# Optimization experiments

Measured on AMD Instinct MI355X. Metric: run time of the kernel, lower is better.

## Reference

```python
import jax, jax.numpy as jnp
import numpy as np
from jax import lax

# ---- fake-quant helpers (brevitas-style per-tensor float scaling, STE round) ----
EPS = 1e-8

def _ste_round(x):
    return x + lax.stop_gradient(jnp.round(x) - x)

def _scale(x, qmax):
    s = lax.stop_gradient(jnp.max(jnp.abs(x))) / qmax
    return jnp.maximum(s, EPS)

def fq(x, scale, qmin, qmax):
    # fake-quantize: round-to-nearest with straight-through estimator, clip, dequant
    return jnp.clip(_ste_round(x / scale), qmin, qmax) * scale

def quant_act_int8(x):
    s = _scale(x, 127.0)
    return fq(x, s, -128.0, 127.0), s

def quant_weight_int4(w):
    # 4-bit signed, narrow range [-7, 7] (brevitas weight quant default narrow_range)
    s = _scale(w, 7.0)
    return fq(w, s, -7.0, 7.0), s

def quant_relu_uint4(x):
    y = jax.nn.relu(x)
    s = _scale(y, 15.0)
    return fq(y, s, 0.0, 15.0)

def quant_bias_int32(b, scale):
    # Int32Bias: bias quantized at input_scale * weight_scale
    return _ste_round(b / scale) * scale

def conv2d_same(x, w):
    # NCHW, OIHW, padding=1, stride=1
    return lax.conv_general_dilated(x, w, window_strides=(1, 1), padding=((1, 1), (1, 1)),
                                    dimension_numbers=('NCHW', 'OIHW', 'NCHW'))

def maxpool2(x):
    return lax.reduce_window(x, -jnp.inf, lax.max, (1, 1, 2, 2), (1, 1, 2, 2), 'VALID')

def quant_conv(x, w, b):
    xq, sx = quant_act_int8(x)        # input_quant: Int8ActPerTensorFloat
    wq, sw = quant_weight_int4(w)     # weight_bit_width=4
    bq = quant_bias_int32(b, sx * sw) # bias_quant: Int32Bias
    y = conv2d_same(xq, wq) + bq[None, :, None, None]
    yq, _ = quant_act_int8(y)         # output_quant: Int8ActPerTensorFloat
    return yq

def quant_linear(x, w, b):
    xq, sx = quant_act_int8(x)
    wq, sw = quant_weight_int4(w)
    bq = quant_bias_int32(b, sx * sw)
    y = xq @ wq.T + bq
    yq, _ = quant_act_int8(y)
    return yq


def setup_inputs() -> dict:
    key = jax.random.key(0)
    ks = jax.random.split(key, 7)
    B = 8192
    x = jax.random.normal(ks[0], (B, 1, 28, 28), dtype=jnp.float32)
    w1 = jax.random.normal(ks[1], (16, 1, 3, 3), dtype=jnp.float32) * 0.3
    b1 = jax.random.normal(ks[2], (16,), dtype=jnp.float32) * 0.1
    w2 = jax.random.normal(ks[3], (32, 16, 3, 3), dtype=jnp.float32) * 0.1
    b2 = jax.random.normal(ks[4], (32,), dtype=jnp.float32) * 0.1
    wf = jax.random.normal(ks[5], (10, 32 * 7 * 7), dtype=jnp.float32) * 0.05
    bf = jax.random.normal(ks[6], (10,), dtype=jnp.float32) * 0.1
    return {'x': x, 'w1': w1, 'b1': b1, 'w2': w2, 'b2': b2, 'wf': wf, 'bf': bf}


def reference(x, w1, b1, w2, b2, wf, bf):
    h, _ = quant_act_int8(x)              # inputQuant
    h = quant_conv(h, w1, b1)             # conv1
    h = quant_relu_uint4(h)               # relu1 (4-bit)
    h = maxpool2(h)                       # pool1 -> [B,16,14,14]
    h = quant_conv(h, w2, b2)             # conv2
    h = quant_relu_uint4(h)               # relu2
    h = maxpool2(h)                       # pool2 -> [B,32,7,7]
    h = h.reshape(h.shape[0], -1)         # flatten -> [B,1568]
    return quant_linear(h, wf, bf)        # fc -> [B,10]
```

## Files before the change

### kernel.cpp

```cpp
#include <hip/hip_runtime.h>
#include <climits>

#define NB 8192
#define EPSQ 1e-8f

using i32x4  = __attribute__((ext_vector_type(4)))  int;
using i32x16 = __attribute__((ext_vector_type(16))) int;

#define WS_F(ws)     ((float*)(ws))
#define WS_I(ws)     ((int*)((char*)(ws)+128))
#define WS_B1L(ws)   ((int*)((char*)(ws)+384))
#define WS_B2L(ws)   ((int*)((char*)(ws)+448))
#define WS_BFL(ws)   ((int*)((char*)(ws)+576))
#define WS_M1F(ws)   ((float*)((char*)(ws)+640))
#define WS_B1F(ws)   ((float*)((char*)(ws)+1280))
#define WS_B2FR(ws)  ((char*)(ws)+2048)
#define WS_Q2TAB(ws) ((signed char*)((char*)(ws)+7168))
#define WS_Q3TAB(ws) ((signed char*)((char*)(ws)+7424))
#define WS_B1FR(ws)  ((char*)(ws)+7680)
#define WS_MFF(ws)   ((float*)((char*)(ws)+20480))
#define WS_WFP(ws)   ((char*)(ws)+83200)
#define WS_RA1(ws)   ((int*)((char*)(ws)+139264))
#define WS_RS1(ws)   ((int*)((char*)(ws)+164352))
#define WS_RA2(ws)   ((int*)((char*)(ws)+189440))
#define WS_RS2(ws)   ((int*)((char*)(ws)+197632))
#define WS_RA3(ws)   ((int*)((char*)(ws)+205824))
#define WS_RAX(ws)   ((float*)((char*)(ws)+206848))
#define WS_WMX(ws)   ((float*)((char*)(ws)+215040))
#define WS_BIG_OFF   217088

__device__ __forceinline__ float clampf(float v, float lo, float hi){ return fminf(fmaxf(v, lo), hi); }

__device__ __forceinline__ float wave_max_f(float v){
#pragma unroll
  for (int off=32; off; off>>=1) v = fmaxf(v, __shfl_down(v, off, 64));
  return v;
}
__device__ __forceinline__ int wave_max_i(int v){
#pragma unroll
  for (int off=32; off; off>>=1) v = max(v, __shfl_down(v, off, 64));
  return v;
}

__device__ __forceinline__ void reduce2_atomic(int amax, int smax, int* gA, int* gS){
  amax = wave_max_i(amax); smax = wave_max_i(smax);
  __shared__ int sA[4], sS[4];
  int w = threadIdx.x>>6, l = threadIdx.x&63;
  if (l==0){ sA[w]=amax; sS[w]=smax; }
  __syncthreads();
  if (threadIdx.x==0){
#pragma unroll
    for (int i=1;i<4;i++){ amax=max(amax,sA[i]); smax=max(smax,sS[i]); }
    atomicMax(gA, amax); atomicMax(gS, smax);
  }
}

__device__ __forceinline__ void reduce2_store(int amax, int smax, int* pA, int* pS){
  amax = wave_max_i(amax); smax = wave_max_i(smax);
  __shared__ int sA[4], sS[4];
  int w = threadIdx.x>>6, l = threadIdx.x&63;
  if (l==0){ sA[w]=amax; sS[w]=smax; }
  __syncthreads();
  if (threadIdx.x==0){
#pragma unroll
    for (int i=1;i<4;i++){ amax=max(amax,sA[i]); smax=max(smax,sS[i]); }
    *pA = amax; *pS = smax;
  }
}

__global__ void k_init(char* ws){
  int* I = WS_I(ws);
  if (threadIdx.x==0){ I[0]=0; I[1]=0; I[2]=INT_MIN; I[3]=0; I[4]=INT_MIN; I[5]=0; }
}

__global__ void k_absx(const float* __restrict__ x, char* ws){
  const float4* x4 = (const float4*)x;
  const int n4 = NB*784/4;
  float m = 0.f;
  for (int i = blockIdx.x*blockDim.x + threadIdx.x; i < n4; i += gridDim.x*blockDim.x){
    float4 v = x4[i];
    m = fmaxf(m, fmaxf(fmaxf(fabsf(v.x),fabsf(v.y)), fmaxf(fabsf(v.z),fabsf(v.w))));
  }
  m = wave_max_f(m);
  __shared__ float sm[4];
  int w = threadIdx.x>>6;
  if ((threadIdx.x&63)==0) sm[w]=m;
  __syncthreads();
  if (threadIdx.x==0){
    m = fmaxf(fmaxf(sm[0],sm[1]), fmaxf(sm[2],sm[3]));
    WS_RAX(ws)[blockIdx.x] = m;
  }
}

__global__ void k_wmax(const float* __restrict__ w1, const float* __restrict__ w2,
                       const float* __restrict__ wf, char* ws){
  __shared__ float red[256];
  int b = blockIdx.x, t = threadIdx.x;
  float m = 0.f;
  if (b==0){ if (t<144) m = fabsf(w1[t]); }
  else if (b<19){ m = fabsf(w2[(b-1)*256 + t]); }
  else { int i=(b-19)*256+t; if (i<15680) m = fabsf(wf[i]); }
  red[t]=m; __syncthreads();
  for (int s=128;s;s>>=1){ if (t<s) red[t]=fmaxf(red[t],red[t+s]); __syncthreads(); }
  if (t==0) WS_WMX(ws)[b]=red[0];
}

__global__ void k_scales(const float* __restrict__ w1, const float* __restrict__ b1, char* ws){
  __shared__ float red[256];
  float* F = WS_F(ws);
  int t = threadIdx.x;
  float vw1 = WS_WMX(ws)[0];
  float m2=0.f, mf=0.f;
  if (t<18) m2 = WS_WMX(ws)[1+t];
  if (t<62) mf = WS_WMX(ws)[19+t];
  red[t]=m2; __syncthreads();
  for (int s=128;s;s>>=1){ if (t<s) red[t]=fmaxf(red[t],red[t+s]); __syncthreads(); }
  float mw2=red[0]; __syncthreads();
  red[t]=mf; __syncthreads();
  for (int s=128;s;s>>=1){ if (t<s) red[t]=fmaxf(red[t],red[t+s]); __syncthreads(); }
  float mwf=red[0]; __syncthreads();
  float mxv=0.f;
  for (int i=t;i<2048;i+=256) mxv=fmaxf(mxv,WS_RAX(ws)[i]);
  red[t]=mxv; __syncthreads();
  for (int s=128;s;s>>=1){ if (t<s) red[t]=fmaxf(red[t],red[t+s]); __syncthreads(); }
  float mx=red[0]; __syncthreads();

  float s0  = fmaxf(mx/127.f, EPSQ);
  float sx1 = fmaxf((127.f*s0)/127.f, EPSQ);
  float sw1 = fmaxf(vw1/7.f, EPSQ);
  float sw2 = fmaxf(mw2/7.f, EPSQ);
  float swf = fmaxf(mwf/7.f, EPSQ);
  float sb1 = sx1*sw1;
  if (t==0){ F[0]=s0; F[1]=sx1; F[2]=sw1; F[3]=sb1; F[7]=sw2; F[12]=swf; }
  if (t<144) WS_M1F(ws)[t] = clampf(rintf(w1[t]/sw1), -7.f, 7.f);
  if (t<16){
    int bl = (int)rintf(b1[t]/sb1);
    WS_B1L(ws)[t] = bl;
    WS_B1F(ws)[t] = (float)bl;
  }
}

__global__ void k_pack(const float* __restrict__ w1, const float* __restrict__ w2,
                       const float* __restrict__ wf, char* ws){
  const float* F = WS_F(ws);
  int id = blockIdx.x*256 + threadIdx.x;
  if (id < 5120){
    float sw2 = F[7];
    int chunk=id>>10, r=id&1023, ln=r>>4, j=r&15;
    int tap=2*chunk+(ln>>5), oc=ln&31;
    signed char v=0;
    if (tap<9) v=(signed char)clampf(rintf(w2[oc*144 + j*9 + tap]/sw2), -7.f, 7.f);
    WS_B2FR(ws)[id]=v;
  } else if (id < 6144){
    float sw1 = F[2];
    int i=id-5120;
    int ln=i>>4, j=i&15;
    int k=(ln>>5)*16+j, oc=ln&31;
    signed char v=0;
    if (k<9 && oc<16) v=(signed char)clampf(rintf(w1[oc*9+k]/sw1), -7.f, 7.f);
    WS_B1FR(ws)[i]=v;
  } else if (id < 56320){
    float swf = F[12];
    int i=id-6144;
    int chunk=i>>10, r2=i&1023, ln=r2>>4, j=r2&15;
    int oc=ln&31, k=chunk*32+(ln>>5)*16+j;
    int cell=k>>5, ch=k&31;
    signed char v=0;
    if (oc<10) v=(signed char)clampf(rintf(wf[oc*1568 + ch*49 + cell]/swf), -7.f, 7.f);
    ((signed char*)WS_WFP(ws))[i]=v;
  } else if (id < 72000){
    float swf = F[12];
    int i=id-56320;
    WS_MFF(ws)[i] = clampf(rintf(wf[i]/swf), -7.f, 7.f);
  }
}

__global__ void k_wq(const float* __restrict__ w1, const float* __restrict__ b1,
                     const float* __restrict__ w2, const float* __restrict__ wf,
                     char* ws){
  __shared__ float red[256];
  float* F = WS_F(ws);
  int t = threadIdx.x;
  auto bmaxabs = [&](const float* p, int n)->float{
    float m=0.f; for (int i=t;i<n;i+=256) m=fmaxf(m,fabsf(p[i]));
    red[t]=m; __syncthreads();
    for (int s=128;s;s>>=1){ if (t<s) red[t]=fmaxf(red[t],red[t+s]); __syncthreads(); }
    float r=red[0]; __syncthreads(); return r;
  };
  float mw1 = bmaxabs(w1,144);
  float mw2 = bmaxabs(w2,4608);
  float mwf = bmaxabs(wf,15680);
  float mxv=0.f;
  for (int i=t;i<2048;i+=256) mxv=fmaxf(mxv,WS_RAX(ws)[i]);
  red[t]=mxv; __syncthreads();
  for (int s=128;s;s>>=1){ if (t<s) red[t]=fmaxf(red[t],red[t+s]); __syncthreads(); }
  float mx=red[0]; __syncthreads();

  float s0  = fmaxf(mx/127.f, EPSQ);
  float sx1 = fmaxf((127.f*s0)/127.f, EPSQ);
  float sw1 = fmaxf(mw1/7.f, EPSQ);
  float sw2 = fmaxf(mw2/7.f, EPSQ);
  float swf = fmaxf(mwf/7.f, EPSQ);
  float sb1 = sx1*sw1;
  if (t==0){ F[0]=s0; F[1]=sx1; F[2]=sw1; F[3]=sb1; F[7]=sw2; F[12]=swf; }
  float* m1f = WS_M1F(ws);
  for (int i=t;i<144;i+=256) m1f[i] = clampf(rintf(w1[i]/sw1), -7.f, 7.f);
  if (t<16){
    int bl = (int)rintf(b1[t]/sb1);
    WS_B1L(ws)[t] = bl;
    WS_B1F(ws)[t] = (float)bl;
  }
  for (int i=t;i<5120;i+=256){
    int chunk=i>>10, r=i&1023, ln=r>>4, j=r&15;
    int tap=2*chunk+(ln>>5), oc=ln&31;
    signed char v=0;
    if (tap<9) v=(signed char)clampf(rintf(w2[oc*144 + j*9 + tap]/sw2), -7.f, 7.f);
    WS_B2FR(ws)[i]=v;
  }
  for (int i=t;i<1024;i+=256){
    int ln=i>>4, j=i&15;
    int k=(ln>>5)*16+j, oc=ln&31;
    signed char v=0;
    if (k<9 && oc<16) v=(signed char)clampf(rintf(w1[oc*9+k]/sw1), -7.f, 7.f);
    WS_B1FR(ws)[i]=v;
  }
  float* mff = WS_MFF(ws);
  for (int i=t;i<15680;i+=256) mff[i] = clampf(rintf(wf[i]/swf), -7.f, 7.f);
  for (int i=t;i<50176;i+=256){
    int chunk=i>>10, r2=i&1023, ln=r2>>4, j=r2&15;
    int oc=ln&31, k=chunk*32+(ln>>5)*16+j;
    int cell=k>>5, ch=k&31;
    signed char v=0;
    if (oc<10) v=(signed char)clampf(rintf(wf[oc*1568 + ch*49 + cell]/swf), -7.f, 7.f);
    ((signed char*)WS_WFP(ws))[i]=v;
  }
}

template<bool FULLR>
__global__ void k_s1(const float* __restrict__ b2, char* ws){
  float* F=WS_F(ws); int* I=WS_I(ws);
  __shared__ int rA[256], rS[256];
  __shared__ float sh[4];
  int t=threadIdx.x;
  int amaxI, smaxI;
  if constexpr (FULLR){
    int a=0, s=INT_MIN;
    const int* ra=WS_RA1(ws); const int* rs=WS_RS1(ws);
    for (int i=t;i<6272;i+=256){ a=max(a,ra[i]); s=max(s,rs[i]); }
    rA[t]=a; rS[t]=s; __syncthreads();
    for (int st=128;st;st>>=1){ if (t<st){ rA[t]=max(rA[t],rA[t+st]); rS[t]=max(rS[t],rS[t+st]); } __syncthreads(); }
    amaxI=rA[0]; smaxI=rS[0];
  } else { amaxI=I[1]; smaxI=I[2]; }
  if (t==0){
    float sb1=F[3];
    float sy1 = fmaxf((sb1*(float)amaxI)/127.f, EPSQ);
    float mp  = sb1*(float)smaxI;
    float P1  = clampf(rintf(mp/sy1), 0.f, 127.f);
    float sr1 = fmaxf((sy1*P1)/15.f, EPSQ);
    float N1  = clampf(rintf((sy1*P1)/sr1), 0.f, 15.f);
    float sx2 = fmaxf((N1*sr1)/127.f, EPSQ);
    float sb2 = sx2*F[7];
    F[4]=sy1; F[5]=sr1; F[6]=sx2; F[8]=sb2;
    sh[0]=sy1; sh[1]=sr1; sh[2]=sx2; sh[3]=sb2;
  }
  __syncthreads();
  float sy1=sh[0], sr1=sh[1], sx2=sh[2], sb2=sh[3];
  int k = t-128;
  float n = (k>0) ? clampf(rintf((sy1*(float)k)/sr1), 0.f, 15.f) : 0.f;
  WS_Q2TAB(ws)[t] = (signed char)clampf(rintf((n*sr1)/sx2), -128.f, 127.f);
  if (t<32) WS_B2L(ws)[t] = (int)rintf(b2[t]/sb2);
}

template<bool FULLR>
__global__ void k_s2(const float* __restrict__ bf, char* ws){
  float* F=WS_F(ws); int* I=WS_I(ws);
  __shared__ int rA[256], rS[256];
  __shared__ float sh[4];
  int t=threadIdx.x;
  int amaxI, smaxI;
  if constexpr (FULLR){
    int a=0, s=INT_MIN;
    const int* ra=WS_RA2(ws); const int* rs=WS_RS2(ws);
    for (int i=t;i<2048;i+=256){ a=max(a,ra[i]); s=max(s,rs[i]); }
    rA[t]=a; rS[t]=s; __syncthreads();
    for (int st=128;st;st>>=1){ if (t<st){ rA[t]=max(rA[t],rA[t+st]); rS[t]=max(rS[t],rS[t+st]); } __syncthreads(); }
    amaxI=rA[0]; smaxI=rS[0];
  } else { amaxI=I[3]; smaxI=I[4]; }
  if (t==0){
    float sb2=F[8];
    float sy2 = fmaxf((sb2*(float)amaxI)/127.f, EPSQ);
    float mp  = sb2*(float)smaxI;
    float P2  = clampf(rintf(mp/sy2), 0.f, 127.f);
    float sr2 = fmaxf((sy2*P2)/15.f, EPSQ);
    float N2  = clampf(rintf((sy2*P2)/sr2), 0.f, 15.f);
    float sx3 = fmaxf((N2*sr2)/127.f, EPSQ);
    float sb3 = sx3*F[12];
    F[9]=sy2; F[10]=sr2; F[11]=sx3; F[13]=sb3;
    sh[0]=sy2; sh[1]=sr2; sh[2]=sx3; sh[3]=sb3;
  }
  __syncthreads();
  float sy2=sh[0], sr2=sh[1], sx3=sh[2], sb3=sh[3];
  int k = t-128;
  float n = (k>0) ? clampf(rintf((sy2*(float)k)/sr2), 0.f, 15.f) : 0.f;
  WS_Q3TAB(ws)[t] = (signed char)clampf(rintf((n*sr2)/sx3), -128.f, 127.f);
  if (t<16) WS_BFL(ws)[t] = (t<10) ? (int)rintf(bf[t]/sb3) : 0;
}

template<bool FULLR>
__global__ void k_s3(char* ws){
  float* F=WS_F(ws); int* I=WS_I(ws);
  __shared__ int rA[256];
  int t=threadIdx.x;
  int amaxI;
  if constexpr (FULLR){
    rA[t] = WS_RA3(ws)[t];
    __syncthreads();
    for (int st=128;st;st>>=1){ if (t<st) rA[t]=max(rA[t],rA[t+st]); __syncthreads(); }
    amaxI = rA[0];
  } else { amaxI = I[5]; }
  if (t==0) F[14] = fmaxf((F[13]*(float)amaxI)/127.f, EPSQ);
}

__global__ void k_qx(const float* __restrict__ x, const char* __restrict__ ws,
                     signed char* __restrict__ qx){
  const float s0 = ((const float*)ws)[0];
  int id = blockIdx.x*256 + threadIdx.x;
  int img = id/240, w = id - img*240;
  int r = w>>3, c4 = (w&7)<<2;
  const float* xi = x + img*784;
  unsigned out = 0;
#pragma unroll
  for (int j=0;j<4;j++){
    int c = c4+j;
    bool valid = (r>=1) && (r<=28) && (c>=1) && (c<=28);
    int q = 0;
    if (valid){
      float xv = xi[(r-1)*28 + (c-1)];
      q = (int)clampf(rintf(xv/s0), -128.f, 127.f);
    }
    out |= ((unsigned)(unsigned char)(signed char)q) << (8*j);
  }
  ((unsigned*)qx)[id] = out;
}

__global__ __launch_bounds__(256) void k_conv1(const signed char* __restrict__ qx,
                                               char* __restrict__ ws,
                                               short* __restrict__ i1p){
  const int t = threadIdx.x;
  const int id = blockIdx.x*256 + t;
  const int img = id/196, cell = id - img*196;
  const int py = cell/14, px = cell - py*14;
  const signed char* qb = qx + img*960 + (2*py)*32;
  const int pc0 = 2*px;
  const int al = pc0 & ~3, sh = (pc0&3)*8;
  float in[4][4];
#pragma unroll
  for (int rr=0; rr<4; rr++){
    unsigned lo = *(const unsigned*)(qb + rr*32 + al);
    unsigned hi = *(const unsigned*)(qb + rr*32 + al + 4);
    unsigned wrd = (unsigned)(((((unsigned long long)hi)<<32)|lo) >> sh);
#pragma unroll
    for (int cc=0; cc<4; cc++)
      in[rr][cc] = (float)(signed char)((wrd >> (8*cc)) & 0xFFu);
  }
  const float* __restrict__ m1f = WS_M1F(ws);
  const float* __restrict__ b1f = WS_B1F(ws);
  int amax=0, smax=INT_MIN;
  short outv[16];
#pragma unroll
  for (int oc=0; oc<16; oc++){
    float b = b1f[oc];
    float a00=b, a01=b, a10=b, a11=b;
#pragma unroll
    for (int dy=0; dy<3; dy++){
#pragma unroll
      for (int dx=0; dx<3; dx++){
        float wt = m1f[oc*9+dy*3+dx];
        a00 = fmaf(in[dy  ][dx  ], wt, a00);
        a01 = fmaf(in[dy  ][dx+1], wt, a01);
        a10 = fmaf(in[dy+1][dx  ], wt, a10);
        a11 = fmaf(in[dy+1][dx+1], wt, a11);
      }
    }
    int v00=(int)a00, v01=(int)a01, v10=(int)a10, v11=(int)a11;
    int mx = max(max(v00,v01), max(v10,v11));
    int ax = max(max(v00<0?-v00:v00, v01<0?-v01:v01), max(v10<0?-v10:v10, v11<0?-v11:v11));
    amax = max(amax, ax);
    smax = max(smax, mx);
    outv[oc] = (short)mx;
  }
  int4* dst = (int4*)(i1p + (size_t)id*16);
  dst[0] = *(const int4*)&outv[0];
  dst[1] = *(const int4*)&outv[8];
  reduce2_store(amax, smax, &WS_RA1(ws)[blockIdx.x], &WS_RS1(ws)[blockIdx.x]);
}

__global__ __launch_bounds__(256) void k_conv2r(char* __restrict__ ws,
                                                short* __restrict__ i1p,
                                                int* __restrict__ p2g){
  __shared__ __align__(16) signed char q2p4[4][4096];
  const int t=threadIdx.x, lane=t&63, wid=t>>6;
  const int img = blockIdx.x*4 + wid;
  signed char* q2p = q2p4[wid];
  const float* F = WS_F(ws);
  const float sb1=F[3], sy1=F[4];
  const signed char* q2t = WS_Q2TAB(ws);

#pragma unroll
  for (int k=0;k<8;k++) ((unsigned long long*)q2p)[lane + 64*k] = 0ULL;

  const unsigned* src = (const unsigned*)(i1p + (size_t)img*3136);
  for (int k=0;k<25;k++){
    int idx = lane + 64*k;
    if (idx >= 1568) break;
    unsigned wv = src[idx];
    int e0 = idx*2;
    int cellc = e0 >> 4, ch = e0 & 15;
    int pyc = cellc/14, pxc = cellc - pyc*14;
    int m0 = (int)(short)(wv & 0xFFFFu);
    int m1 = (int)(short)(wv >> 16);
    float k10 = clampf(rintf((sb1*(float)m0)/sy1), -128.f, 127.f);
    float k11 = clampf(rintf((sb1*(float)m1)/sy1), -128.f, 127.f);
    int b0 = (int)(unsigned char)q2t[(int)k10+128];
    int b1 = (int)(unsigned char)q2t[(int)k11+128];
    *(unsigned short*)(q2p + ((pyc+1)*16 + (pxc+1))*16 + ch) = (unsigned short)(b0 | (b1<<8));
  }

  i32x4 bfr[5];
  const i32x4* bg = (const i32x4*)WS_B2FR(ws);
#pragma unroll
  for (int c=0;c<5;c++) bfr[c] = bg[c*64+lane];
  const int col = lane&31, h = lane>>5;
  const int bias = WS_B2L(ws)[col];
  int amax2=0, smax2=INT_MIN;
  const int TOFF[9] = {0,1,2,16,17,18,32,33,34};
  int* dstb = p2g + (size_t)img*1568;

#pragma unroll
  for (int mt=0; mt<7; mt++){
    int m = mt*32 + col;
    int g = m>>2, sub = m&3;
    bool gv = g < 49;
    int py = (g*37)>>8;
    int px = g - py*7;
    int oy = 2*py + (sub>>1), ox = 2*px + (sub&1);
    int E0 = oy*16 + ox;
    i32x16 acc;
#pragma unroll
    for (int r=0;r<16;r++) acc[r] = bias;
#pragma unroll
    for (int c=0;c<5;c++){
      const int t0 = TOFF[2*c];
      const int t1 = (2*c+1<9) ? TOFF[2*c+1] : -1;
      int toff = h ? t1 : t0;
      int entry = (gv && toff>=0) ? (E0 + toff) : 0;
      i32x4 a = *(const i32x4*)(q2p + entry*16);
      acc = __builtin_amdgcn_mfma_i32_32x32x32_i8(a, bfr[c], acc, 0,0,0);
    }
#pragma unroll
    for (int i=0;i<4;i++){
      int gg = mt*8 + 2*i + h;
      if (gg < 49){
        int v0=acc[4*i], v1=acc[4*i+1], v2=acc[4*i+2], v3=acc[4*i+3];
        int a0=v0<0?-v0:v0, a1=v1<0?-v1:v1, a2=v2<0?-v2:v2, a3=v3<0?-v3:v3;
        amax2 = max(amax2, max(max(a0,a1),max(a2,a3)));
        int mx = max(max(v0,v1),max(v2,v3));
        smax2 = max(smax2, mx);
        dstb[gg*32 + col] = mx;
      }
    }
  }
  reduce2_store(amax2, smax2, &WS_RA2(ws)[blockIdx.x], &WS_RS2(ws)[blockIdx.x]);
}

__global__ void k_rq2(const char* __restrict__ ws, const int* __restrict__ p2g,
                      signed char* __restrict__ q3g){
  const float* F = (const float*)ws;
  const float sb2 = F[8], sy2 = F[9];
  const signed char* q3t = WS_Q3TAB(ws);
  int id = blockIdx.x*256 + threadIdx.x;
  i32x4 m4 = ((const i32x4*)p2g)[id];
  unsigned out=0;
#pragma unroll
  for (int j=0;j<4;j++){
    float k2 = clampf(rintf((sb2*(float)m4[j])/sy2), -128.f, 127.f);
    out |= ((unsigned)(unsigned char)q3t[(int)k2+128]) << (8*j);
  }
  ((unsigned*)q3g)[id] = out;
}

__global__ __launch_bounds__(256) void k_fc(char* __restrict__ ws,
                                            const signed char* __restrict__ q3g,
                                            int* __restrict__ i3out){
  __shared__ int part[3][16][64];
  int t=threadIdx.x, lane=t&63, wid=t>>6;
  int mt = blockIdx.x;
  const int col=lane&31, h=lane>>5;
  const signed char* A0 = q3g + (size_t)(mt*32 + col)*1568 + 16*h;
  const i32x4* wfp = (const i32x4*)WS_WFP(ws);
  i32x16 acc;
#pragma unroll
  for (int r=0;r<16;r++) acc[r]=0;
  for (int c=wid; c<49; c+=4){
    i32x4 a = *(const i32x4*)(A0 + c*32);
    i32x4 b = wfp[c*64 + lane];
    acc = __builtin_amdgcn_mfma_i32_32x32x32_i8(a, b, acc, 0,0,0);
  }
  if (wid>0){
#pragma unroll
    for (int r=0;r<16;r++) part[wid-1][r][lane] = acc[r];
  }
  __syncthreads();
  if (wid==0){
    int bias = (col<10) ? WS_BFL(ws)[col] : 0;
    int am=0;
#pragma unroll
    for (int r=0;r<16;r++){
      int v = acc[r] + part[0][r][lane] + part[1][r][lane] + part[2][r][lane] + bias;
      int row=(r&3)+8*(r>>2)+4*h;
      int img = mt*32+row;
      if (col<10){
        i3out[img*10+col] = v;
        am = max(am, v<0?-v:v);
      }
    }
    am = wave_max_i(am);
    if (lane==0) WS_RA3(ws)[blockIdx.x] = am;
  }
}

__global__ __launch_bounds__(256) void k_c1(const float* __restrict__ x, char* __restrict__ ws,
                                            short* __restrict__ i1p){
  constexpr int OFF_K0=0, OFF_A=960, OFF_I1=13760, OFF_B1=38848;
  __shared__ __align__(16) char arena[38912];
  signed char* k0b = (signed char*)(arena+OFF_K0);
  signed char* Abuf= (signed char*)(arena+OFF_A);
  short*       I1s = (short*)(arena+OFF_I1);
  int*         b1i = (int*)(arena+OFF_B1);

  const int tid=threadIdx.x, img=blockIdx.x;
  const int lane=tid&63, wid=tid>>6;
  const float s0 = WS_F(ws)[0];

  if (tid<16) b1i[tid]=WS_B1L(ws)[tid];
  for (int i=tid;i<240;i+=256) ((int*)k0b)[i]=0;
  for (int i=tid;i<3200;i+=256) ((int*)Abuf)[i]=0;
  __syncthreads();
  const float* xi = x + img*784;
  for (int i=tid;i<784;i+=256){
    int r=i/28, c=i-r*28;
    float v = clampf(rintf(xi[i]/s0), -128.f, 127.f);
    k0b[(r+1)*32 + (c+1)] = (signed char)v;
  }
  __syncthreads();
  for (int p=tid;p<784;p+=256){
    int oy=p/28, ox=p-oy*28;
    int base = oy*32+ox;
    int al = base & ~3, sh = (base&3)*8;
    unsigned l0a=*(const unsigned*)(k0b+al),    l1a=*(const unsigned*)(k0b+al+4);
    unsigned l0b=*(const unsigned*)(k0b+al+32), l1b=*(const unsigned*)(k0b+al+36);
    unsigned l0c=*(const unsigned*)(k0b+al+64), l1c=*(const unsigned*)(k0b+al+68);
    unsigned u0=(unsigned)(((((unsigned long long)l1a)<<32)|l0a)>>sh);
    unsigned u1=(unsigned)(((((unsigned long long)l1b)<<32)|l0b)>>sh);
    unsigned u2=(unsigned)(((((unsigned long long)l1c)<<32)|l0c)>>sh);
    i32x4 row;
    row[0]=(int)((u0&0xFFFFFFu)|(u1<<24));
    row[1]=(int)(((u1>>8)&0xFFFFu)|((u2&0xFFFFu)<<16));
    row[2]=(int)((u2>>16)&0xFFu);
    row[3]=0;
    *(i32x4*)(Abuf + p*16) = row;
  }
  __syncthreads();
  const i32x4 bfr = ((const i32x4*)WS_B1FR(ws))[lane];
  const int col=lane&31, h=lane>>5;
  const int bias=(col<16)? b1i[col] : 0;
  int amax=0, smax=INT_MIN;
  for (int mt=wid; mt<25; mt+=4){
    i32x4 a={0,0,0,0};
    if (h==0) a = *(const i32x4*)(Abuf + (mt*32+col)*16);
    i32x16 acc;
#pragma unroll
    for (int r=0;r<16;r++) acc[r]=bias;
    acc=__builtin_amdgcn_mfma_i32_32x32x32_i8(a,bfr,acc,0,0,0);
#pragma unroll
    for (int r=0;r<16;r++){
      int row=(r&3)+8*(r>>2)+4*h;
      int p=mt*32+row;
      if (p<784 && col<16){
        int v=acc[r];
        amax=max(amax,v<0?-v:v); smax=max(smax,v);
        I1s[p*16+col]=(short)v;
      }
    }
  }
  __syncthreads();
  for (int i=tid;i<3136;i+=256){
    int pp=i>>4, c=i&15, py=pp/14, px=pp-py*14;
    int p0=py*56+px*2;
    int m=max(max((int)I1s[p0*16+c],(int)I1s[(p0+1)*16+c]),
              max((int)I1s[(p0+28)*16+c],(int)I1s[(p0+29)*16+c]));
    i1p[(size_t)img*3136 + i]=(short)m;
  }
  reduce2_atomic(amax,smax,&WS_I(ws)[1],&WS_I(ws)[2]);
}

template<bool FIN>
__global__ __launch_bounds__(256) void k_c2(char* __restrict__ ws, const short* __restrict__ i1p,
                                            int* __restrict__ i3out){
  constexpr int OFF_Q2L=0, OFF_B2I=3136, OFF_Q2T=3264, OFF_N2=3520,
                OFF_Q3T=9792, OFF_BFS=10048, OFF_Q3F=10112, OFF_RED=16384;
  constexpr int ARENA = FIN ? 16544 : 3520;
  __shared__ __align__(16) char arena[ARENA];
  signed char* q2l=(signed char*)(arena+OFF_Q2L);
  int* b2li=(int*)(arena+OFF_B2I);
  signed char* q2t=(signed char*)(arena+OFF_Q2T);

  const int tid=threadIdx.x, img=blockIdx.x;
  const int lane=tid&63, wid=tid>>6;
  const float* F=WS_F(ws);
  const float sb1=F[3], sy1=F[4];

  q2t[tid]=WS_Q2TAB(ws)[tid];
  if (tid<32) b2li[tid]=WS_B2L(ws)[tid];
  if constexpr (FIN){
    ((signed char*)(arena+OFF_Q3T))[tid]=WS_Q3TAB(ws)[tid];
    if (tid<16) ((int*)(arena+OFF_BFS))[tid]=WS_BFL(ws)[tid];
  }
  __syncthreads();
  for (int i=tid;i<3136;i+=256){
    int m=(int)i1p[(size_t)img*3136+i];
    float k1=clampf(rintf((sb1*(float)m)/sy1),-128.f,127.f);
    q2l[i]=q2t[(int)k1+128];
  }
  __syncthreads();

  i32x4 bfr[5];
  {
    const i32x4* bg=(const i32x4*)WS_B2FR(ws);
#pragma unroll
    for (int c=0;c<5;c++) bfr[c]=bg[c*64+lane];
  }
  const int col=lane&31, h=lane>>5;
  const int bias=b2li[col];
  int amax2=0, smax2=INT_MIN;
  float sb2=0.f, sy2=0.f;
  signed char* n2buf=nullptr;
  if constexpr (FIN){ sb2=F[8]; sy2=F[9]; n2buf=(signed char*)(arena+OFF_N2); }

  for (int mt=wid; mt<7; mt+=4){
    const int p=mt*32+col;
    const bool pv=p<196;
    const int oy=p/14, ox=p-oy*14;
    i32x16 acc;
#pragma unroll
    for (int r=0;r<16;r++) acc[r]=bias;
#pragma unroll
    for (int c=0;c<5;c++){
      const int tap=2*c+h;
      i32x4 a={0,0,0,0};
      if (pv && tap<9){
        const int iy=oy+tap/3-1, ix=ox+tap-(tap/3)*3-1;
        if ((unsigned)iy<14u && (unsigned)ix<14u) a=*(const i32x4*)(q2l+(iy*14+ix)*16);
      }
      acc=__builtin_amdgcn_mfma_i32_32x32x32_i8(a,bfr[c],acc,0,0,0);
    }
#pragma unroll
    for (int r=0;r<16;r++){
      const int row=(r&3)+8*(r>>2)+4*h;
      const int pp=mt*32+row;
      if (pp<196){
        const int v=acc[r];
        if constexpr (!FIN){ amax2=max(amax2,v<0?-v:v); smax2=max(smax2,v); }
        else {
          n2buf[col*196+pp]=(signed char)clampf(rintf((sb2*(float)v)/sy2),-128.f,127.f);
        }
      }
    }
  }
  if constexpr (!FIN){
    reduce2_atomic(amax2,smax2,&WS_I(ws)[3],&WS_I(ws)[4]);
    return;
  } else {
    __syncthreads();
    signed char* q3t_s=(signed char*)(arena+OFF_Q3T);
    float* q3f=(float*)(arena+OFF_Q3F);
    for (int i=tid;i<1568;i+=256){
      int cch=i/49, s=i-cch*49, qy=s/7, qx=s-qy*7;
      int b=cch*196+qy*28+qx*2;
      int m=max(max((int)n2buf[b],(int)n2buf[b+1]),max((int)n2buf[b+14],(int)n2buf[b+15]));
      q3f[i]=(float)q3t_s[m+128];
    }
    __syncthreads();
    const float* mff=WS_MFF(ws);
    float a10[10];
#pragma unroll
    for (int o=0;o<10;o++) a10[o]=0.f;
    for (int k=tid;k<1568;k+=256){
      float qa=q3f[k];
#pragma unroll
      for (int o=0;o<10;o++) a10[o]=fmaf(qa,mff[o*1568+k],a10[o]);
    }
#pragma unroll
    for (int o=0;o<10;o++){
#pragma unroll
      for (int off=32;off;off>>=1) a10[o]+=__shfl_down(a10[o],off,64);
    }
    float* redf=(float*)(arena+OFF_RED);
    int* bfs=(int*)(arena+OFF_BFS);
    if (lane==0){
#pragma unroll
      for (int o=0;o<10;o++) redf[wid*10+o]=a10[o];
    }
    __syncthreads();
    if (tid<10){
      float s=redf[tid]+redf[10+tid]+redf[20+tid]+redf[30+tid];
      int I3v=(int)s+bfs[tid];
      i3out[img*10+tid]=I3v;
      redf[tid]=(float)(I3v<0?-I3v:I3v);
    }
    __syncthreads();
    if (tid==0){
      int m=0;
#pragma unroll
      for (int o=0;o<10;o++) m=max(m,(int)redf[o]);
      atomicMax(&WS_I(ws)[5],m);
    }
  }
}

__global__ void k_out(char* ws, float* __restrict__ out){
  float* F=WS_F(ws);
  float sb3=F[13], sy3=F[14];
  int i = blockIdx.x*blockDim.x + threadIdx.x;
  if (i < NB*10){
    int iv = ((const int*)out)[i];
    float y = sb3*(float)iv;
    float q = clampf(rintf(y/sy3), -128.f, 127.f);
    out[i] = q*sy3;
  }
}

extern "C" void kernel_launch(void* const* d_in, const int* in_sizes, int n_in,
                              void* d_out, int out_size, void* d_ws, size_t ws_size,
                              hipStream_t stream){
  const float* x  = (const float*)d_in[0];
  const float* w1 = (const float*)d_in[1];
  const float* b1 = (const float*)d_in[2];
  const float* w2 = (const float*)d_in[3];
  const float* b2 = (const float*)d_in[4];
  const float* wf = (const float*)d_in[5];
  const float* bf = (const float*)d_in[6];
  char* ws = (char*)d_ws;
  float* out = (float*)d_out;
  int* i3 = (int*)d_out;

  const size_t QX_SZ  = (size_t)NB*960;
  const size_t I1_SZ  = (size_t)NB*6272;
  const size_t Q3_SZ  = (size_t)NB*1568;
  const size_t needFull = (size_t)WS_BIG_OFF + QX_SZ + I1_SZ + Q3_SZ;

  if (ws_size >= needFull){
    signed char* qx  = (signed char*)(ws + WS_BIG_OFF);
    short*       i1p = (short*)(ws + WS_BIG_OFF + QX_SZ);
    int*         p2g = (int*)i1p;
    signed char* q3g = (signed char*)(ws + WS_BIG_OFF + QX_SZ + I1_SZ);
    k_absx  <<<dim3(2048), dim3(256), 0, stream>>>(x, ws);
    k_wmax  <<<dim3(81), dim3(256), 0, stream>>>(w1, w2, wf, ws);
    k_scales<<<dim3(1), dim3(256), 0, stream>>>(w1, b1, ws);
    k_qx    <<<dim3(NB*240/256), dim3(256), 0, stream>>>(x, ws, qx);
    k_pack  <<<dim3(282), dim3(256), 0, stream>>>(w1, w2, wf, ws);
    k_conv1 <<<dim3(NB*196/256), dim3(256), 0, stream>>>(qx, ws, i1p);
    k_s1<true><<<dim3(1), dim3(256), 0, stream>>>(b2, ws);
    k_conv2r<<<dim3(NB/4), dim3(256), 0, stream>>>(ws, i1p, p2g);
    k_s2<true><<<dim3(1), dim3(256), 0, stream>>>(bf, ws);
    k_rq2   <<<dim3(NB*1568/1024), dim3(256), 0, stream>>>(ws, p2g, q3g);
    k_fc    <<<dim3(256), dim3(256), 0, stream>>>(ws, q3g, i3);
    k_s3<true><<<dim3(1), dim3(256), 0, stream>>>(ws);
  } else {
    short* i1p = (short*)(ws + WS_BIG_OFF);
    k_init<<<dim3(1), dim3(64), 0, stream>>>(ws);
    k_absx<<<dim3(2048), dim3(256), 0, stream>>>(x, ws);
    k_wq  <<<dim3(1), dim3(256), 0, stream>>>(w1, b1, w2, wf, ws);
    k_c1<<<dim3(NB), dim3(256), 0, stream>>>(x, ws, i1p);
    k_s1<false><<<dim3(1), dim3(256), 0, stream>>>(b2, ws);
    k_c2<false><<<dim3(NB), dim3(256), 0, stream>>>(ws, i1p, i3);
    k_s2<false><<<dim3(1), dim3(256), 0, stream>>>(bf, ws);
    k_c2<true ><<<dim3(NB), dim3(256), 0, stream>>>(ws, i1p, i3);
    k_s3<false><<<dim3(1), dim3(256), 0, stream>>>(ws);
  }
  k_out<<<dim3((NB*10+255)/256), dim3(256), 0, stream>>>(ws, out);
}
```

Measured before the change: 137.8 us.

## Fuse conv2 requant into FC, precompute int16 requant LUT, merge s3 into output

Adds a 64K-entry table that maps each possible int16 pooled conv1 value directly to its conv2 input byte, so conv2r does one lookup per element instead of float math plus a lookup. The separate requantize pass (k_rq2) is folded into the FC kernel, which requantizes its 32 images' pooled conv2 outputs into shared memory before the MFMA loop. This removes a global int8 intermediate buffer and one launch. The final scale reduction (k_s3) is merged into the output kernel, where every block redundantly reduces the 256 partial maxima. The cost is that the FC kernel now reads int32 data through a serial per-image loop and uses about 50KB of shared memory, which can lower occupancy.

```diff
diff --git a/kernel.cpp b/kernel.cpp
--- a/kernel.cpp
+++ b/kernel.cpp
@@ -27,7 +27,8 @@
 #define WS_RA3(ws)   ((int*)((char*)(ws)+205824))
 #define WS_RAX(ws)   ((float*)((char*)(ws)+206848))
 #define WS_WMX(ws)   ((float*)((char*)(ws)+215040))
-#define WS_BIG_OFF   217088
+#define WS_Q2B(ws)   ((signed char*)((char*)(ws)+215552))
+#define WS_BIG_OFF   281600
 
 __device__ __forceinline__ float clampf(float v, float lo, float hi){ return fminf(fmaxf(v, lo), hi); }
 
@@ -271,6 +272,15 @@
   if (t<32) WS_B2L(ws)[t] = (int)rintf(b2[t]/sb2);
 }
 
+__global__ void k_q2big(char* ws){
+  const float* F = WS_F(ws);
+  const float sb1=F[3], sy1=F[4];
+  int idx = blockIdx.x*256 + threadIdx.x;
+  int m = idx - 32768;
+  float k1 = clampf(rintf((sb1*(float)m)/sy1), -128.f, 127.f);
+  WS_Q2B(ws)[idx] = WS_Q2TAB(ws)[(int)k1+128];
+}
+
 template<bool FULLR>
 __global__ void k_s2(const float* __restrict__ bf, char* ws){
   float* F=WS_F(ws); int* I=WS_I(ws);
@@ -402,9 +412,7 @@
   const int t=threadIdx.x, lane=t&63, wid=t>>6;
   const int img = blockIdx.x*4 + wid;
   signed char* q2p = q2p4[wid];
-  const float* F = WS_F(ws);
-  const float sb1=F[3], sy1=F[4];
-  const signed char* q2t = WS_Q2TAB(ws);
+  const signed char* __restrict__ q2b = WS_Q2B(ws);
 
 #pragma unroll
   for (int k=0;k<8;k++) ((unsigned long long*)q2p)[lane + 64*k] = 0ULL;
@@ -419,10 +427,8 @@
     int pyc = cellc/14, pxc = cellc - pyc*14;
     int m0 = (int)(short)(wv & 0xFFFFu);
     int m1 = (int)(short)(wv >> 16);
-    float k10 = clampf(rintf((sb1*(float)m0)/sy1), -128.f, 127.f);
-    float k11 = clampf(rintf((sb1*(float)m1)/sy1), -128.f, 127.f);
-    int b0 = (int)(unsigned char)q2t[(int)k10+128];
-    int b1 = (int)(unsigned char)q2t[(int)k11+128];
+    int b0 = (int)(unsigned char)q2b[m0+32768];
+    int b1 = (int)(unsigned char)q2b[m1+32768];
     *(unsigned short*)(q2p + ((pyc+1)*16 + (pxc+1))*16 + ch) = (unsigned short)(b0 | (b1<<8));
   }
 
@@ -473,36 +479,32 @@
   reduce2_store(amax2, smax2, &WS_RA2(ws)[blockIdx.x], &WS_RS2(ws)[blockIdx.x]);
 }
 
-__global__ void k_rq2(const char* __restrict__ ws, const int* __restrict__ p2g,
-                      signed char* __restrict__ q3g){
-  const float* F = (const float*)ws;
+__global__ __launch_bounds__(256) void k_fc2(char* __restrict__ ws,
+                                             const int* __restrict__ p2g,
+                                             int* __restrict__ i3out){
+  __shared__ __align__(16) signed char q3l[32*1584];
+  __shared__ int part[3][16][64];
+  const float* F = WS_F(ws);
   const float sb2 = F[8], sy2 = F[9];
-  const signed char* q3t = WS_Q3TAB(ws);
-  int id = blockIdx.x*256 + threadIdx.x;
-  i32x4 m4 = ((const i32x4*)p2g)[id];
-  unsigned out=0;
-#pragma unroll
-  for (int j=0;j<4;j++){
-    float k2 = clampf(rintf((sb2*(float)m4[j])/sy2), -128.f, 127.f);
-    out |= ((unsigned)(unsigned char)q3t[(int)k2+128]) << (8*j);
-  }
-  ((unsigned*)q3g)[id] = out;
-}
-
-__global__ __launch_bounds__(256) void k_fc(char* __restrict__ ws,
-                                            const signed char* __restrict__ q3g,
-                                            int* __restrict__ i3out){
-  __shared__ int part[3][16][64];
+  const signed char* __restrict__ q3t = WS_Q3TAB(ws);
   int t=threadIdx.x, lane=t&63, wid=t>>6;
   int mt = blockIdx.x;
+  const int* pb = p2g + (size_t)mt*32*1568;
+  for (int il=0; il<32; il++){
+    for (int k=t; k<1568; k+=256){
+      int v = pb[il*1568 + k];
+      float k2 = clampf(rintf((sb2*(float)v)/sy2), -128.f, 127.f);
+      q3l[il*1584 + k] = q3t[(int)k2+128];
+    }
+  }
+  __syncthreads();
   const int col=lane&31, h=lane>>5;
-  const signed char* A0 = q3g + (size_t)(mt*32 + col)*1568 + 16*h;
   const i32x4* wfp = (const i32x4*)WS_WFP(ws);
   i32x16 acc;
 #pragma unroll
   for (int r=0;r<16;r++) acc[r]=0;
   for (int c=wid; c<49; c+=4){
-    i32x4 a = *(const i32x4*)(A0 + c*32);
+    i32x4 a = *(const i32x4*)(q3l + col*1584 + 16*h + c*32);
     i32x4 b = wfp[c*64 + lane];
     acc = __builtin_amdgcn_mfma_i32_32x32x32_i8(a, b, acc, 0,0,0);
   }
@@ -526,6 +528,23 @@
     }
     am = wave_max_i(am);
     if (lane==0) WS_RA3(ws)[blockIdx.x] = am;
+  }
+}
+
+__global__ void k_out2(char* __restrict__ ws, float* __restrict__ out){
+  __shared__ int rA[256];
+  int t=threadIdx.x;
+  rA[t] = WS_RA3(ws)[t];
+  __syncthreads();
+  for (int st=128;st;st>>=1){ if (t<st) rA[t]=max(rA[t],rA[t+st]); __syncthreads(); }
+  float sb3 = WS_F(ws)[13];
+  float sy3 = fmaxf((sb3*(float)rA[0])/127.f, EPSQ);
+  int i = blockIdx.x*256 + t;
+  if (i < NB*10){
+    int iv = ((const int*)out)[i];
+    float y = sb3*(float)iv;
+    float q = clampf(rintf(y/sy3), -128.f, 127.f);
+    out[i] = q*sy3;
   }
 }
 
@@ -756,14 +775,12 @@
 
   const size_t QX_SZ  = (size_t)NB*960;
   const size_t I1_SZ  = (size_t)NB*6272;
-  const size_t Q3_SZ  = (size_t)NB*1568;
-  const size_t needFull = (size_t)WS_BIG_OFF + QX_SZ + I1_SZ + Q3_SZ;
+  const size_t needFull = (size_t)WS_BIG_OFF + QX_SZ + I1_SZ;
 
   if (ws_size >= needFull){
     signed char* qx  = (signed char*)(ws + WS_BIG_OFF);
     short*       i1p = (short*)(ws + WS_BIG_OFF + QX_SZ);
     int*         p2g = (int*)i1p;
-    signed char* q3g = (signed char*)(ws + WS_BIG_OFF + QX_SZ + I1_SZ);
     k_absx  <<<dim3(2048), dim3(256), 0, stream>>>(x, ws);
     k_wmax  <<<dim3(81), dim3(256), 0, stream>>>(w1, w2, wf, ws);
     k_scales<<<dim3(1), dim3(256), 0, stream>>>(w1, b1, ws);
@@ -771,11 +788,11 @@
     k_pack  <<<dim3(282), dim3(256), 0, stream>>>(w1, w2, wf, ws);
     k_conv1 <<<dim3(NB*196/256), dim3(256), 0, stream>>>(qx, ws, i1p);
     k_s1<true><<<dim3(1), dim3(256), 0, stream>>>(b2, ws);
+    k_q2big <<<dim3(256), dim3(256), 0, stream>>>(ws);
     k_conv2r<<<dim3(NB/4), dim3(256), 0, stream>>>(ws, i1p, p2g);
     k_s2<true><<<dim3(1), dim3(256), 0, stream>>>(bf, ws);
-    k_rq2   <<<dim3(NB*1568/1024), dim3(256), 0, stream>>>(ws, p2g, q3g);
-    k_fc    <<<dim3(256), dim3(256), 0, stream>>>(ws, q3g, i3);
-    k_s3<true><<<dim3(1), dim3(256), 0, stream>>>(ws);
+    k_fc2   <<<dim3(256), dim3(256), 0, stream>>>(ws, p2g, i3);
+    k_out2  <<<dim3((NB*10+255)/256), dim3(256), 0, stream>>>(ws, out);
   } else {
     short* i1p = (short*)(ws + WS_BIG_OFF);
     k_init<<<dim3(1), dim3(64), 0, stream>>>(ws);
@@ -787,6 +804,6 @@
     k_s2<false><<<dim3(1), dim3(256), 0, stream>>>(bf, ws);
     k_c2<true ><<<dim3(NB), dim3(256), 0, stream>>>(ws, i1p, i3);
     k_s3<false><<<dim3(1), dim3(256), 0, stream>>>(ws);
-  }
-  k_out<<<dim3((NB*10+255)/256), dim3(256), 0, stream>>>(ws, out);
-}
+    k_out<<<dim3((NB*10+255)/256), dim3(256), 0, stream>>>(ws, out);
+  }
+}
```

New measurement: 222.4 us. +61.4%, slower.
